# Kernel tuning notes

Measured on AMD Instinct MI355X. Metric: run time of the kernel, lower is better.

## Reference

```python
import jax, jax.numpy as jnp
import numpy as np

E = 8      # num_experts
A = 128    # angle feature size = input_size - 4
TGT = 3    # target size
HID = 16   # expert MLP hidden / latent / main GRU hidden
OUT = 128  # motion decoder output size
B = 64
W = 128
F = A + TGT + 1  # 132
BN_EPS = 1e-5


def _gru_layer(x, Wih, Whh, bih, bhh):
    # x: (B, T, I); Wih: (3H, I); Whh: (3H, H). PyTorch GRU equations.
    xW = jnp.einsum('bti,gi->btg', x, Wih) + bih  # precompute input gates (B,T,3H)
    H = Whh.shape[1]

    def step(h, xw):
        gh = h @ Whh.T + bhh
        ir, iz, inn = jnp.split(xw, 3, axis=-1)
        hr, hz, hn = jnp.split(gh, 3, axis=-1)
        r = jax.nn.sigmoid(ir + hr)
        z = jax.nn.sigmoid(iz + hz)
        n = jnp.tanh(inn + r * hn)
        h_new = (1.0 - z) * n + z * h
        return h_new, h_new

    h0 = jnp.zeros((x.shape[0], H), x.dtype)
    _, ys = jax.lax.scan(step, h0, jnp.swapaxes(xW, 0, 1))
    return jnp.swapaxes(ys, 0, 1)  # (B, T, H)


def _expert_mlp(x, om, w1, b1, w2, b2, g, bt):
    # Blend expert weights per-sample, then matvec; fused as one einsum (same math).
    h = jnp.einsum('bi,be,eih->bh', x, om, w1) + om @ b1
    # BatchNorm1d, training-mode batch statistics (biased variance), then ELU
    m = h.mean(0)
    v = h.var(0)
    h = jax.nn.elu(g * (h - m) * jax.lax.rsqrt(v + BN_EPS) + bt)
    return jnp.einsum('bh,be,eho->bo', h, om, w2) + om @ b2


def _forward(Local, Remote,
             gW_ih0, gW_hh0, gb_ih0, gb_hh0, gW_ih1, gW_hh1, gb_ih1, gb_hh1,
             ae_w1, ae_b1, ae_w2, ae_b2, ae_g, ae_bt,
             md_w1, md_b1, md_w2, md_b2, md_g, md_bt,
             mW_ih0, mW_hh0, mb_ih0, mb_hh0, mW_ih1, mW_hh1, mb_ih1, mb_hh1):
    Bn, Wn, _ = Local.shape
    LA = Local[..., :A]
    RA = Remote[..., :A]
    LT = Local[..., A:A + TGT]
    RT = Remote[..., A:A + TGT]
    Scale = Remote[..., A + TGT]  # (B, W)

    def gate(t):
        h = _gru_layer(t, gW_ih0, gW_hh0, gb_ih0, gb_hh0)
        h = _gru_layer(h, gW_ih1, gW_hh1, gb_ih1, gb_hh1)
        return jax.nn.softmax(h, axis=-1)

    Lo = gate(LT)  # (B, W, E)
    Ro = gate(RT)

    ZL = _expert_mlp(LA.reshape(-1, A), Lo.reshape(-1, E), ae_w1, ae_b1, ae_w2, ae_b2, ae_g, ae_bt)
    ZR = _expert_mlp(RA.reshape(-1, A), Ro.reshape(-1, E), ae_w1, ae_b1, ae_w2, ae_b2, ae_g, ae_bt)
    Z = (ZL + ZR).reshape(Bn, Wn, HID)

    Z = _gru_layer(Z, mW_ih0, mW_hh0, mb_ih0, mb_hh0)
    Z = _gru_layer(Z, mW_ih1, mW_hh1, mb_ih1, mb_hh1)
    Z = Z[:, -1]  # (B, HID)

    dec_in = jnp.concatenate([Z, Scale[:, -1:]], axis=-1)  # (B, HID+1)
    return _expert_mlp(dec_in, Ro[:, -1], md_w1, md_b1, md_w2, md_b2, md_g, md_bt)


def setup_inputs() -> dict:
    key = jax.random.key(0)
    ks = iter(jax.random.split(key, 40))

    def u(shape, bound):
        return jax.random.uniform(next(ks), shape, jnp.float32, -bound, bound)

    d = {}
    d['Local'] = jax.random.normal(next(ks), (B, W, F), jnp.float32)
    d['Remote'] = jax.random.normal(next(ks), (B, W, F), jnp.float32)

    def gru_params(pref, isz, hsz):
        bd = 1.0 / np.sqrt(hsz)
        d[pref + 'W_ih0'] = u((3 * hsz, isz), bd)
        d[pref + 'W_hh0'] = u((3 * hsz, hsz), bd)
        d[pref + 'b_ih0'] = u((3 * hsz,), bd)
        d[pref + 'b_hh0'] = u((3 * hsz,), bd)
        d[pref + 'W_ih1'] = u((3 * hsz, hsz), bd)
        d[pref + 'W_hh1'] = u((3 * hsz, hsz), bd)
        d[pref + 'b_ih1'] = u((3 * hsz,), bd)
        d[pref + 'b_hh1'] = u((3 * hsz,), bd)

    gru_params('g', TGT, E)    # gating GRU: 2 layers, hidden = num_experts
    gru_params('m', HID, HID)  # main GRU: 2 layers, hidden = 16

    def expert(pref, isz, hsz, osz):
        b1 = float(np.sqrt(6.0 / (isz * hsz)))
        b2 = float(np.sqrt(6.0 / (hsz * osz)))
        d[pref + '_w1'] = u((E, isz, hsz), b1)
        d[pref + '_b1'] = jnp.zeros((E, hsz), jnp.float32)
        d[pref + '_w2'] = u((E, hsz, osz), b2)
        d[pref + '_b2'] = jnp.zeros((E, osz), jnp.float32)
        d[pref + '_g'] = jnp.ones((hsz,), jnp.float32)
        d[pref + '_bt'] = jnp.zeros((hsz,), jnp.float32)

    expert('ae', A, HID, HID)        # angle encoder
    expert('md', HID + 1, HID, OUT)  # motion decoder
    return d


def reference(Local, Remote,
              gW_ih0, gW_hh0, gb_ih0, gb_hh0, gW_ih1, gW_hh1, gb_ih1, gb_hh1,
              ae_w1, ae_b1, ae_w2, ae_b2, ae_g, ae_bt,
              md_w1, md_b1, md_w2, md_b2, md_g, md_bt,
              mW_ih0, mW_hh0, mb_ih0, mb_hh0, mW_ih1, mW_hh1, mb_ih1, mb_hh1):
    return _forward(Local, Remote,
                    gW_ih0, gW_hh0, gb_ih0, gb_hh0, gW_ih1, gW_hh1, gb_ih1, gb_hh1,
                    ae_w1, ae_b1, ae_w2, ae_b2, ae_g, ae_bt,
                    md_w1, md_b1, md_w2, md_b2, md_g, md_bt,
                    mW_ih0, mW_hh0, mb_ih0, mb_hh0, mW_ih1, mW_hh1, mb_ih1, mb_hh1)
```

## Files before the change

kernel.cpp:

```cpp
#include <hip/hip_runtime.h>
#include <cstdint>
#include <cstddef>

#define DEV __device__ __forceinline__

typedef float v2f __attribute__((ext_vector_type(2)));

DEV float fsig(float x)  { return __builtin_amdgcn_rcpf(1.0f + __expf(-x)); }
DEV float ftanh_(float x){ return 1.0f - 2.0f * __builtin_amdgcn_rcpf(1.0f + __expf(2.0f * x)); }
DEV float readlanef(float v, int l) {
    return __uint_as_float(__builtin_amdgcn_readlane(__float_as_uint(v), l));
}
DEV v2f fma2v(v2f a, float b, v2f c) {
    return (v2f){ fmaf(a.x, b, c.x), fmaf(a.y, b, c.y) };
}

constexpr size_t ACC   = 0;
constexpr size_t LO    = 128;
constexpr size_t RO    = LO + 65536;
constexpr size_t HBUF  = RO + 65536;
constexpr size_t XW0   = HBUF + 262144;
constexpr size_t ZLAST = XW0 + 393216;

__global__ __launch_bounds__(64) void k1_gate(
    const float* __restrict__ Local, const float* __restrict__ Remote,
    const float* __restrict__ Wih0, const float* __restrict__ Whh0,
    const float* __restrict__ bih0, const float* __restrict__ bhh0,
    const float* __restrict__ Wih1, const float* __restrict__ Whh1,
    const float* __restrict__ bih1, const float* __restrict__ bhh1,
    float* __restrict__ ws)
{
    const int tid = threadIdx.x;
    const int j = tid & 7;
    const int layer = (tid >> 3) & 1;
    const int blk = blockIdx.x;
    const int track = blk >> 6;
    const int b = blk & 63;
    if (blk == 0) ws[ACC + tid] = 0.f;

    __shared__ float xwg[128][24];
    __shared__ float h1all[128][9];

    const float* __restrict__ src = track ? Remote : Local;
    for (int t = tid; t < 128; t += 64) {
        const float* p = src + ((size_t)b * 128 + t) * 132 + 128;
        float x0 = p[0], x1 = p[1], x2 = p[2];
#pragma unroll
        for (int u = 0; u < 24; ++u) {
            float a = bih0[u];
            a = fmaf(Wih0[u * 3 + 0], x0, a);
            a = fmaf(Wih0[u * 3 + 1], x1, a);
            a = fmaf(Wih0[u * 3 + 2], x2, a);
            xwg[t][u] = a;
        }
    }

    v2f wrz[16], wnn[16];
    float base_r, base_z, base_in, base_dn;
    if (layer == 0) {
#pragma unroll
        for (int k = 0; k < 8; ++k) {
            wrz[k] = (v2f){ Whh0[j * 8 + k], Whh0[(8 + j) * 8 + k] };
            wnn[k] = (v2f){ 0.f, Whh0[(16 + j) * 8 + k] };
            wrz[8 + k] = (v2f){0.f, 0.f};
            wnn[8 + k] = (v2f){0.f, 0.f};
        }
        base_r = bhh0[j];
        base_z = bhh0[8 + j];
        base_in = 0.f;
        base_dn = bhh0[16 + j];
    } else {
#pragma unroll
        for (int k = 0; k < 8; ++k) {
            wrz[k] = (v2f){ Wih1[j * 8 + k], Wih1[(8 + j) * 8 + k] };
            wnn[k] = (v2f){ Wih1[(16 + j) * 8 + k], 0.f };
            wrz[8 + k] = (v2f){ Whh1[j * 8 + k], Whh1[(8 + j) * 8 + k] };
            wnn[8 + k] = (v2f){ 0.f, Whh1[(16 + j) * 8 + k] };
        }
        base_r = bih1[j] + bhh1[j];
        base_z = bih1[8 + j] + bhh1[8 + j];
        base_in = bih1[16 + j];
        base_dn = bhh1[16 + j];
    }
    const float m0f = (layer == 0) ? 1.f : 0.f;
    __syncthreads();

    float hown = 0.f;
    float p0 = xwg[0][j], p1 = xwg[0][8 + j], p2 = xwg[0][16 + j];
#pragma unroll 1
    for (int t = 0; t <= 128; ++t) {
        int tn = t < 127 ? t + 1 : 127;
        float q0 = xwg[tn][j], q1 = xwg[tn][8 + j], q2 = xwg[tn][16 + j];
        float vb[16];
#pragma unroll
        for (int k = 0; k < 16; ++k) vb[k] = readlanef(hown, k);
        v2f arz = (v2f){ fmaf(m0f, p0, base_r), fmaf(m0f, p1, base_z) };
        v2f ann = (v2f){ fmaf(m0f, p2, base_in), base_dn };
#pragma unroll
        for (int k = 0; k < 16; ++k) {
            arz = fma2v(wrz[k], vb[k], arz);
            ann = fma2v(wnn[k], vb[k], ann);
        }
        float r = fsig(arz.x);
        float z = fsig(arz.y);
        float n = ftanh_(ann.x + r * ann.y);
        float hnew = (1.f - z) * n + z * hown;
        bool act = layer ? (t >= 1) : (t < 128);
        hown = act ? hnew : hown;
        if (tid >= 8 && tid < 16 && t >= 1) h1all[t - 1][j] = hown;
        p0 = q0; p1 = q1; p2 = q2;
    }
    __syncthreads();

    float* __restrict__ outp = ws + (track ? RO : LO);
    for (int t = tid; t < 128; t += 64) {
        float vv[8];
#pragma unroll
        for (int k = 0; k < 8; ++k) vv[k] = h1all[t][k];
        float mx = vv[0];
#pragma unroll
        for (int k = 1; k < 8; ++k) mx = fmaxf(mx, vv[k]);
        float ssum = 0.f;
#pragma unroll
        for (int k = 0; k < 8; ++k) { vv[k] = __expf(vv[k] - mx); ssum += vv[k]; }
        float inv = __builtin_amdgcn_rcpf(ssum);
        size_t base = ((size_t)b * 128 + t) * 8;
        float4 o0 = make_float4(vv[0] * inv, vv[1] * inv, vv[2] * inv, vv[3] * inv);
        float4 o1 = make_float4(vv[4] * inv, vv[5] * inv, vv[6] * inv, vv[7] * inv);
        *(float4*)(outp + base) = o0;
        *(float4*)(outp + base + 4) = o1;
    }
}

__global__ __launch_bounds__(256) void k2_expert1(
    const float* __restrict__ Local, const float* __restrict__ Remote,
    const float* __restrict__ ae_w1, const float* __restrict__ ae_b1,
    float* __restrict__ ws)
{
    const int blk = blockIdx.x;
    const int track = blk >> 7;
    const int n0 = (blk & 127) * 64;
    const float* __restrict__ X = track ? Remote : Local;
    const float* __restrict__ om = ws + (track ? RO : LO);

    __shared__ __align__(16) float xsh[64 * 132];
    __shared__ __align__(16) float wsh[16 * 1040];
    __shared__ float omsh[64][8];
    __shared__ float b1sh[128];
    __shared__ float red[32];
    const int tid = threadIdx.x;

    for (int i = tid; i < 2048; i += 256) {
        int r = i >> 5, q = i & 31;
        ((float4*)&xsh[r * 132])[q] = ((const float4*)(X + (size_t)(n0 + r) * 132))[q];
    }
    for (int i4 = tid; i4 < 4096; i4 += 256) {
        float4 v = ((const float4*)ae_w1)[i4];
        int i = i4 * 4;
#pragma unroll
        for (int c = 0; c < 4; ++c) {
            int ii = i + c;
            int h = ii & 15, kk = (ii >> 4) & 127, e = ii >> 11;
            float vc = c == 0 ? v.x : c == 1 ? v.y : c == 2 ? v.z : v.w;
            wsh[h * 1040 + e * 130 + kk] = vc;
        }
    }
    for (int i = tid; i < 512; i += 256) omsh[i >> 3][i & 7] = om[(size_t)(n0 + (i >> 3)) * 8 + (i & 7)];
    for (int i = tid; i < 128; i += 256) b1sh[i] = ae_b1[i];
    if (tid < 32) red[tid] = 0.f;
    __syncthreads();

    const int hh = tid & 15, rg = tid >> 4;
    float acc[4][8];
#pragma unroll
    for (int r = 0; r < 4; ++r)
#pragma unroll
        for (int e = 0; e < 8; ++e) acc[r][e] = 0.f;

#pragma unroll 4
    for (int kq = 0; kq < 32; ++kq) {
        float4 xv[4], wv[8];
#pragma unroll
        for (int r = 0; r < 4; ++r) xv[r] = *(const float4*)&xsh[(rg * 4 + r) * 132 + kq * 4];
#pragma unroll
        for (int e = 0; e < 8; ++e) wv[e] = *(const float4*)&wsh[hh * 1040 + e * 130 + kq * 4];
#pragma unroll
        for (int r = 0; r < 4; ++r)
#pragma unroll
            for (int e = 0; e < 8; ++e) {
                float a = acc[r][e];
                a = fmaf(xv[r].x, wv[e].x, a);
                a = fmaf(xv[r].y, wv[e].y, a);
                a = fmaf(xv[r].z, wv[e].z, a);
                a = fmaf(xv[r].w, wv[e].w, a);
                acc[r][e] = a;
            }
    }

    float s = 0.f, s2 = 0.f;
    float* __restrict__ hout = ws + HBUF + (size_t)track * 131072;
#pragma unroll
    for (int r = 0; r < 4; ++r) {
        int row = rg * 4 + r;
        float hv = 0.f;
#pragma unroll
        for (int e = 0; e < 8; ++e) hv = fmaf(omsh[row][e], acc[r][e] + b1sh[e * 16 + hh], hv);
        hout[(size_t)(n0 + row) * 16 + hh] = hv;
        s += hv; s2 += hv * hv;
    }
    __syncthreads();
    atomicAdd(&red[hh], s);
    atomicAdd(&red[16 + hh], s2);
    __syncthreads();
    if (tid < 32) atomicAdd(&ws[ACC + track * 32 + tid], red[tid]);
}

__global__ __launch_bounds__(256) void k3_bn_mlp2(
    const float* __restrict__ ae_w2, const float* __restrict__ ae_b2,
    const float* __restrict__ ae_g, const float* __restrict__ ae_bt,
    const float* __restrict__ mWih0, const float* __restrict__ mbih0,
    float* __restrict__ ws)
{
    const int n0 = blockIdx.x * 64;
    const int tid = threadIdx.x;
    __shared__ float actsh[2][64][16];
    __shared__ float omsh[2][64][8];
    __shared__ float w2sh[2048];
    __shared__ float b2sh[128];
    __shared__ float zsh[64][17];
    __shared__ float wihsh[48][17];
    __shared__ float bihsh[48];
    __shared__ float stat[4][16];

    if (tid < 32) {
        int trk = tid >> 4, h = tid & 15;
        float s = ws[ACC + trk * 32 + h], s2 = ws[ACC + trk * 32 + 16 + h];
        float m = s * (1.f / 8192.f);
        float v = fmaxf(s2 * (1.f / 8192.f) - m * m, 0.f);
        stat[trk * 2][h] = m;
        stat[trk * 2 + 1][h] = rsqrtf(v + 1e-5f);
    }
    for (int i = tid; i < 2048; i += 256) w2sh[i] = ae_w2[i];
    for (int i = tid; i < 128; i += 256) b2sh[i] = ae_b2[i];
    for (int i = tid; i < 768; i += 256) wihsh[i >> 4][i & 15] = mWih0[i];
    if (tid < 48) bihsh[tid] = mbih0[tid];
    for (int i = tid; i < 1024; i += 256) {
        int trk = i >> 9, r = (i >> 3) & 63, e = i & 7;
        omsh[trk][r][e] = ws[(trk ? RO : LO) + (size_t)(n0 + r) * 8 + e];
    }
    __syncthreads();

    for (int i = tid; i < 2048; i += 256) {
        int trk = i >> 10, r = (i >> 4) & 63, h = i & 15;
        float v = ws[HBUF + (size_t)trk * 131072 + (size_t)(n0 + r) * 16 + h];
        float a = ae_g[h] * (v - stat[trk * 2][h]) * stat[trk * 2 + 1][h] + ae_bt[h];
        actsh[trk][r][h] = a > 0.f ? a : expm1f(a);
    }
    __syncthreads();

    for (int i = tid; i < 1024; i += 256) {
        int r = i >> 4, o = i & 15;
        float accv = 0.f;
#pragma unroll
        for (int trk = 0; trk < 2; ++trk) {
#pragma unroll
            for (int e = 0; e < 8; ++e) {
                const float* w = &w2sh[e * 256 + o];
                float t = b2sh[e * 16 + o];
#pragma unroll
                for (int h = 0; h < 16; ++h) t = fmaf(actsh[trk][r][h], w[h * 16], t);
                accv = fmaf(omsh[trk][r][e], t, accv);
            }
        }
        zsh[r][o] = accv;
    }
    __syncthreads();

    for (int i = tid; i < 3072; i += 256) {
        int r = i / 48, gr = i - r * 48;
        float a = bihsh[gr];
#pragma unroll
        for (int k = 0; k < 16; ++k) a = fmaf(zsh[r][k], wihsh[gr][k], a);
        ws[XW0 + (size_t)(n0 + r) * 48 + gr] = a;
    }
}

__global__ __launch_bounds__(64) void k4_maingru(
    const float* __restrict__ Whh0, const float* __restrict__ bhh0,
    const float* __restrict__ Wih1, const float* __restrict__ Whh1,
    const float* __restrict__ bih1, const float* __restrict__ bhh1,
    float* __restrict__ ws)
{
    const int tid = threadIdx.x;
    const int j = tid & 15;
    const int layer = (tid >> 4) & 1;
    const int seq = blockIdx.x;

    __shared__ __align__(16) float4 xw4[1536];
    float* xwsh = (float*)xw4;

    const float4* __restrict__ xsrc = (const float4*)(ws + XW0 + (size_t)seq * 6144);
    for (int i = tid; i < 1536; i += 64) xw4[i] = xsrc[i];

    v2f wrz[32], wnn[32];
    float base_r, base_z, base_in, base_dn;
    if (layer == 0) {
#pragma unroll
        for (int k = 0; k < 16; ++k) {
            wrz[k] = (v2f){ Whh0[j * 16 + k], Whh0[(16 + j) * 16 + k] };
            wnn[k] = (v2f){ 0.f, Whh0[(32 + j) * 16 + k] };
            wrz[16 + k] = (v2f){0.f, 0.f};
            wnn[16 + k] = (v2f){0.f, 0.f};
        }
        base_r = bhh0[j];
        base_z = bhh0[16 + j];
        base_in = 0.f;
        base_dn = bhh0[32 + j];
    } else {
#pragma unroll
        for (int k = 0; k < 16; ++k) {
            wrz[k] = (v2f){ Wih1[j * 16 + k], Wih1[(16 + j) * 16 + k] };
            wnn[k] = (v2f){ Wih1[(32 + j) * 16 + k], 0.f };
            wrz[16 + k] = (v2f){ Whh1[j * 16 + k], Whh1[(16 + j) * 16 + k] };
            wnn[16 + k] = (v2f){ 0.f, Whh1[(32 + j) * 16 + k] };
        }
        base_r = bih1[j] + bhh1[j];
        base_z = bih1[16 + j] + bhh1[16 + j];
        base_in = bih1[32 + j];
        base_dn = bhh1[32 + j];
    }
    const float m0f = (layer == 0) ? 1.f : 0.f;
    __syncthreads();

    float hown = 0.f;
    float p0 = xwsh[j], p1 = xwsh[16 + j], p2 = xwsh[32 + j];
#pragma unroll 1
    for (int t = 0; t <= 128; ++t) {
        int tn = (t < 127 ? t + 1 : 127) * 48;
        float q0 = xwsh[tn + j], q1 = xwsh[tn + 16 + j], q2 = xwsh[tn + 32 + j];
        float vb[32];
#pragma unroll
        for (int k = 0; k < 32; ++k) vb[k] = readlanef(hown, k);
        v2f arz = (v2f){ fmaf(m0f, p0, base_r), fmaf(m0f, p1, base_z) };
        v2f ann = (v2f){ fmaf(m0f, p2, base_in), base_dn };
#pragma unroll
        for (int k = 0; k < 32; ++k) {
            arz = fma2v(wrz[k], vb[k], arz);
            ann = fma2v(wnn[k], vb[k], ann);
        }
        float r = fsig(arz.x);
        float z = fsig(arz.y);
        float n = ftanh_(ann.x + r * ann.y);
        float hnew = (1.f - z) * n + z * hown;
        bool act = layer ? (t >= 1) : (t < 128);
        hown = act ? hnew : hown;
        p0 = q0; p1 = q1; p2 = q2;
    }
    if (tid >= 16 && tid < 32) ws[ZLAST + (size_t)seq * 16 + j] = hown;
}

__global__ __launch_bounds__(256) void k5_dec(
    const float* __restrict__ Remote,
    const float* __restrict__ md_w1, const float* __restrict__ md_b1,
    const float* __restrict__ md_g, const float* __restrict__ md_bt,
    const float* __restrict__ md_w2, const float* __restrict__ md_b2,
    const float* __restrict__ ws, float* __restrict__ out)
{
    const int o0 = blockIdx.x * 8;
    const int tid = threadIdx.x;
    __shared__ float xsh[64][17];
    __shared__ float omsh[64][8];
    __shared__ float w1sh[2176];
    __shared__ float b1sh[128];
    __shared__ float hsh[64][17];
    __shared__ float ssum[16], ss2[16], mstat[2][16];
    __shared__ float ash[64][17];
    __shared__ float w2sh[8][16][8];
    __shared__ float b2sh[8][8];

    for (int i = tid; i < 1024; i += 256) xsh[i >> 4][i & 15] = ws[ZLAST + i];
    if (tid < 64) xsh[tid][16] = Remote[((size_t)tid * 128 + 127) * 132 + 131];
    for (int i = tid; i < 512; i += 256)
        omsh[i >> 3][i & 7] = ws[RO + ((size_t)(i >> 3) * 128 + 127) * 8 + (i & 7)];
    for (int i = tid; i < 2176; i += 256) w1sh[i] = md_w1[i];
    for (int i = tid; i < 128; i += 256) b1sh[i] = md_b1[i];
    for (int i = tid; i < 1024; i += 256) {
        int e = i >> 7, h = (i >> 3) & 15, oo = i & 7;
        w2sh[e][h][oo] = md_w2[((size_t)e * 16 + h) * 128 + o0 + oo];
    }
    if (tid < 64) b2sh[tid >> 3][tid & 7] = md_b2[(size_t)(tid >> 3) * 128 + o0 + (tid & 7)];
    if (tid < 16) { ssum[tid] = 0.f; ss2[tid] = 0.f; }
    __syncthreads();

    for (int i = tid; i < 1024; i += 256) {
        int b = i >> 4, h = i & 15;
        float accv = 0.f;
#pragma unroll
        for (int e = 0; e < 8; ++e) {
            float t = b1sh[e * 16 + h];
            const float* w = &w1sh[e * 272 + h];
#pragma unroll
            for (int i2 = 0; i2 < 17; ++i2) t = fmaf(xsh[b][i2], w[i2 * 16], t);
            accv = fmaf(omsh[b][e], t, accv);
        }
        hsh[b][h] = accv;
        atomicAdd(&ssum[h], accv);
        atomicAdd(&ss2[h], accv * accv);
    }
    __syncthreads();
    if (tid < 16) {
        float m = ssum[tid] * (1.f / 64.f);
// ... 9 lines not shown
    }
    __syncthreads();

    for (int i = tid; i < 512; i += 256) {
        int b = i >> 3, oo = i & 7;
        float accv = 0.f;
#pragma unroll
        for (int e = 0; e < 8; ++e) {
            float t = b2sh[e][oo];
#pragma unroll
            for (int h = 0; h < 16; ++h) t = fmaf(ash[b][h], w2sh[e][h][oo], t);
            accv = fmaf(omsh[b][e], t, accv);
        }
        out[(size_t)b * 128 + o0 + oo] = accv;
    }
}

extern "C" void kernel_launch(void* const* d_in, const int* in_sizes, int n_in,
                              void* d_out, int out_size, void* d_ws, size_t ws_size,
                              hipStream_t stream) {
    const float* Local  = (const float*)d_in[0];
    const float* Remote = (const float*)d_in[1];
    const float* gWih0  = (const float*)d_in[2];
    const float* gWhh0  = (const float*)d_in[3];
    const float* gbih0  = (const float*)d_in[4];
    const float* gbhh0  = (const float*)d_in[5];
    const float* gWih1  = (const float*)d_in[6];
    const float* gWhh1  = (const float*)d_in[7];
    const float* gbih1  = (const float*)d_in[8];
    const float* gbhh1  = (const float*)d_in[9];
    const float* mWih0  = (const float*)d_in[10];
    const float* mWhh0  = (const float*)d_in[11];
    const float* mbih0  = (const float*)d_in[12];
    const float* mbhh0  = (const float*)d_in[13];
    const float* mWih1  = (const float*)d_in[14];
    const float* mWhh1  = (const float*)d_in[15];
    const float* mbih1  = (const float*)d_in[16];
    const float* mbhh1  = (const float*)d_in[17];
    const float* ae_w1  = (const float*)d_in[18];
    const float* ae_b1  = (const float*)d_in[19];
    const float* ae_w2  = (const float*)d_in[20];
    const float* ae_b2  = (const float*)d_in[21];
    const float* ae_g   = (const float*)d_in[22];
    const float* ae_bt  = (const float*)d_in[23];
    const float* md_w1  = (const float*)d_in[24];
    const float* md_b1  = (const float*)d_in[25];
    const float* md_w2  = (const float*)d_in[26];
    const float* md_b2  = (const float*)d_in[27];
    const float* md_g   = (const float*)d_in[28];
    const float* md_bt  = (const float*)d_in[29];
    float* ws  = (float*)d_ws;
    float* out = (float*)d_out;

    k1_gate<<<128, 64, 0, stream>>>(Local, Remote, gWih0, gWhh0, gbih0, gbhh0,
                                    gWih1, gWhh1, gbih1, gbhh1, ws);
    k2_expert1<<<256, 256, 0, stream>>>(Local, Remote, ae_w1, ae_b1, ws);
    k3_bn_mlp2<<<128, 256, 0, stream>>>(ae_w2, ae_b2, ae_g, ae_bt, mWih0, mbih0, ws);
    k4_maingru<<<64, 64, 0, stream>>>(mWhh0, mbhh0, mWih1, mWhh1, mbih1, mbhh1, ws);
    k5_dec<<<16, 256, 0, stream>>>(Remote, md_w1, md_b1, md_g, md_bt,
                                   md_w2, md_b2, ws, out);
}
```

Before: 264.9 us.

## Fuse BN/expert-MLP2 with main GRU and split GRU dot products into independent chains

Merges the BatchNorm/ELU/second expert layer and input-gate projection kernel with the main GRU recurrence kernel, so each block computes its sequence's input gates directly into shared memory instead of round-tripping through global workspace, removing one launch. The GRU inner loops in both the gate and main GRU kernels replace packed v2f accumulators with six scalar FMA chains split by half of the hidden vector, shortening dependency chains on the serial critical path. The fused kernel uses only 64 of 256 threads for the recurrence and needs more shared memory per block, and only 64 blocks do the MLP work that 128 blocks did before.

```diff
diff --git a/kernel.cpp b/kernel.cpp
--- a/kernel.cpp
+++ b/kernel.cpp
@@ -3,26 +3,20 @@
 #include <cstddef>
 
 #define DEV __device__ __forceinline__
-
-typedef float v2f __attribute__((ext_vector_type(2)));
 
 DEV float fsig(float x)  { return __builtin_amdgcn_rcpf(1.0f + __expf(-x)); }
 DEV float ftanh_(float x){ return 1.0f - 2.0f * __builtin_amdgcn_rcpf(1.0f + __expf(2.0f * x)); }
 DEV float readlanef(float v, int l) {
     return __uint_as_float(__builtin_amdgcn_readlane(__float_as_uint(v), l));
 }
-DEV v2f fma2v(v2f a, float b, v2f c) {
-    return (v2f){ fmaf(a.x, b, c.x), fmaf(a.y, b, c.y) };
-}
 
 constexpr size_t ACC   = 0;
 constexpr size_t LO    = 128;
 constexpr size_t RO    = LO + 65536;
 constexpr size_t HBUF  = RO + 65536;
-constexpr size_t XW0   = HBUF + 262144;
-constexpr size_t ZLAST = XW0 + 393216;
-
-__global__ __launch_bounds__(64) void k1_gate(
+constexpr size_t ZLAST = HBUF + 262144;
+
+__global__ __launch_bounds__(64, 1) void k1_gate(
     const float* __restrict__ Local, const float* __restrict__ Remote,
     const float* __restrict__ Wih0, const float* __restrict__ Whh0,
     const float* __restrict__ bih0, const float* __restrict__ bhh0,
@@ -55,34 +49,23 @@
         }
     }
 
-    v2f wrz[16], wnn[16];
-    float base_r, base_z, base_in, base_dn;
-    if (layer == 0) {
-#pragma unroll
-        for (int k = 0; k < 8; ++k) {
-            wrz[k] = (v2f){ Whh0[j * 8 + k], Whh0[(8 + j) * 8 + k] };
-            wnn[k] = (v2f){ 0.f, Whh0[(16 + j) * 8 + k] };
-            wrz[8 + k] = (v2f){0.f, 0.f};
-            wnn[8 + k] = (v2f){0.f, 0.f};
-        }
-        base_r = bhh0[j];
-        base_z = bhh0[8 + j];
-        base_in = 0.f;
-        base_dn = bhh0[16 + j];
-    } else {
-#pragma unroll
-        for (int k = 0; k < 8; ++k) {
-            wrz[k] = (v2f){ Wih1[j * 8 + k], Wih1[(8 + j) * 8 + k] };
-            wnn[k] = (v2f){ Wih1[(16 + j) * 8 + k], 0.f };
-            wrz[8 + k] = (v2f){ Whh1[j * 8 + k], Whh1[(8 + j) * 8 + k] };
-            wnn[8 + k] = (v2f){ 0.f, Whh1[(16 + j) * 8 + k] };
-        }
-        base_r = bih1[j] + bhh1[j];
-        base_z = bih1[8 + j] + bhh1[8 + j];
-        base_in = bih1[16 + j];
-        base_dn = bhh1[16 + j];
-    }
-    const float m0f = (layer == 0) ? 1.f : 0.f;
+    const float* __restrict__ Wlo = layer ? Wih1 : Whh0;
+    const float mhi = layer ? 1.f : 0.f;
+    const float m0f = layer ? 0.f : 1.f;
+    float wr[16], wz[16], wc[16];
+#pragma unroll
+    for (int k = 0; k < 8; ++k) {
+        wr[k] = Wlo[j * 8 + k];
+        wz[k] = Wlo[(8 + j) * 8 + k];
+        wc[k] = Wlo[(16 + j) * 8 + k];
+        wr[8 + k] = mhi * Whh1[j * 8 + k];
+        wz[8 + k] = mhi * Whh1[(8 + j) * 8 + k];
+        wc[8 + k] = mhi * Whh1[(16 + j) * 8 + k];
+    }
+    const float base_r  = layer ? (bih1[j] + bhh1[j])         : bhh0[j];
+    const float base_z  = layer ? (bih1[8 + j] + bhh1[8 + j]) : bhh0[8 + j];
+    const float base_in = layer ? bih1[16 + j]                : 0.f;
+    const float base_dn = layer ? bhh1[16 + j]                : bhh0[16 + j];
     __syncthreads();
 
     float hown = 0.f;
@@ -94,16 +77,24 @@
         float vb[16];
 #pragma unroll
         for (int k = 0; k < 16; ++k) vb[k] = readlanef(hown, k);
-        v2f arz = (v2f){ fmaf(m0f, p0, base_r), fmaf(m0f, p1, base_z) };
-        v2f ann = (v2f){ fmaf(m0f, p2, base_in), base_dn };
-#pragma unroll
-        for (int k = 0; k < 16; ++k) {
-            arz = fma2v(wrz[k], vb[k], arz);
-            ann = fma2v(wnn[k], vb[k], ann);
-        }
-        float r = fsig(arz.x);
-        float z = fsig(arz.y);
-        float n = ftanh_(ann.x + r * ann.y);
+        float ar_a = fmaf(m0f, p0, base_r), ar_b = 0.f;
+        float az_a = fmaf(m0f, p1, base_z), az_b = 0.f;
+        float ac_lo = 0.f, ac_hi = 0.f;
+#pragma unroll
+        for (int k = 0; k < 8; ++k) {
+            ar_a  = fmaf(wr[k], vb[k], ar_a);
+            az_a  = fmaf(wz[k], vb[k], az_a);
+            ac_lo = fmaf(wc[k], vb[k], ac_lo);
+            ar_b  = fmaf(wr[8 + k], vb[8 + k], ar_b);
+            az_b  = fmaf(wz[8 + k], vb[8 + k], az_b);
+            ac_hi = fmaf(wc[8 + k], vb[8 + k], ac_hi);
+        }
+        float r = fsig(ar_a + ar_b);
+        float z = fsig(az_a + az_b);
+        float tin = base_in + ac_lo;
+        float in_ = layer ? tin : p2;
+        float dn  = base_dn + (layer ? ac_hi : ac_lo);
+        float n = ftanh_(in_ + r * dn);
         float hnew = (1.f - z) * n + z * hown;
         bool act = layer ? (t >= 1) : (t < 128);
         hown = act ? hnew : hown;
@@ -215,122 +206,103 @@
     if (tid < 32) atomicAdd(&ws[ACC + track * 32 + tid], red[tid]);
 }
 
-__global__ __launch_bounds__(256) void k3_bn_mlp2(
+__global__ __launch_bounds__(256, 1) void k34_fused(
     const float* __restrict__ ae_w2, const float* __restrict__ ae_b2,
     const float* __restrict__ ae_g, const float* __restrict__ ae_bt,
     const float* __restrict__ mWih0, const float* __restrict__ mbih0,
-    float* __restrict__ ws)
-{
-    const int n0 = blockIdx.x * 64;
-    const int tid = threadIdx.x;
-    __shared__ float actsh[2][64][16];
-    __shared__ float omsh[2][64][8];
-    __shared__ float w2sh[2048];
-    __shared__ float b2sh[128];
-    __shared__ float zsh[64][17];
-    __shared__ float wihsh[48][17];
-    __shared__ float bihsh[48];
-    __shared__ float stat[4][16];
-
-    if (tid < 32) {
-        int trk = tid >> 4, h = tid & 15;
-        float s = ws[ACC + trk * 32 + h], s2 = ws[ACC + trk * 32 + 16 + h];
-        float m = s * (1.f / 8192.f);
-        float v = fmaxf(s2 * (1.f / 8192.f) - m * m, 0.f);
-        stat[trk * 2][h] = m;
-        stat[trk * 2 + 1][h] = rsqrtf(v + 1e-5f);
-    }
-    for (int i = tid; i < 2048; i += 256) w2sh[i] = ae_w2[i];
-    for (int i = tid; i < 128; i += 256) b2sh[i] = ae_b2[i];
-    for (int i = tid; i < 768; i += 256) wihsh[i >> 4][i & 15] = mWih0[i];
-    if (tid < 48) bihsh[tid] = mbih0[tid];
-    for (int i = tid; i < 1024; i += 256) {
-        int trk = i >> 9, r = (i >> 3) & 63, e = i & 7;
-        omsh[trk][r][e] = ws[(trk ? RO : LO) + (size_t)(n0 + r) * 8 + e];
-    }
-    __syncthreads();
-
-    for (int i = tid; i < 2048; i += 256) {
-        int trk = i >> 10, r = (i >> 4) & 63, h = i & 15;
-        float v = ws[HBUF + (size_t)trk * 131072 + (size_t)(n0 + r) * 16 + h];
-        float a = ae_g[h] * (v - stat[trk * 2][h]) * stat[trk * 2 + 1][h] + ae_bt[h];
-        actsh[trk][r][h] = a > 0.f ? a : expm1f(a);
-    }
-    __syncthreads();
-
-    for (int i = tid; i < 1024; i += 256) {
-        int r = i >> 4, o = i & 15;
-        float accv = 0.f;
-#pragma unroll
-        for (int trk = 0; trk < 2; ++trk) {
-#pragma unroll
-            for (int e = 0; e < 8; ++e) {
-                const float* w = &w2sh[e * 256 + o];
-                float t = b2sh[e * 16 + o];
-#pragma unroll
-                for (int h = 0; h < 16; ++h) t = fmaf(actsh[trk][r][h], w[h * 16], t);
-                accv = fmaf(omsh[trk][r][e], t, accv);
-            }
-        }
-        zsh[r][o] = accv;
-    }
-    __syncthreads();
-
-    for (int i = tid; i < 3072; i += 256) {
-        int r = i / 48, gr = i - r * 48;
-        float a = bihsh[gr];
-#pragma unroll
-        for (int k = 0; k < 16; ++k) a = fmaf(zsh[r][k], wihsh[gr][k], a);
-        ws[XW0 + (size_t)(n0 + r) * 48 + gr] = a;
-    }
-}
-
-__global__ __launch_bounds__(64) void k4_maingru(
     const float* __restrict__ Whh0, const float* __restrict__ bhh0,
     const float* __restrict__ Wih1, const float* __restrict__ Whh1,
     const float* __restrict__ bih1, const float* __restrict__ bhh1,
     float* __restrict__ ws)
 {
+    const int s = blockIdx.x;
     const int tid = threadIdx.x;
+
+    __shared__ float stat[4][16];
+    __shared__ float omsh[2][128][8];
+    __shared__ float w2sh[2048];
+    __shared__ float b2sh[128];
+    __shared__ float actsh[2][128][16];
+    __shared__ float zsh[128][17];
+    __shared__ float wihsh[48][17];
+    __shared__ float bihsh[48];
+    __shared__ float xwsh[128 * 48];
+
+    if (tid < 32) {
+        int trk = tid >> 4, h = tid & 15;
+        float sm = ws[ACC + trk * 32 + h], s2 = ws[ACC + trk * 32 + 16 + h];
+        float m = sm * (1.f / 8192.f);
+        float v = fmaxf(s2 * (1.f / 8192.f) - m * m, 0.f);
+        stat[trk * 2][h] = m;
+        stat[trk * 2 + 1][h] = rsqrtf(v + 1e-5f);
+    }
+    for (int i = tid; i < 2048; i += 256) w2sh[i] = ae_w2[i];
+    for (int i = tid; i < 128; i += 256) b2sh[i] = ae_b2[i];
+    for (int i = tid; i < 768; i += 256) wihsh[i >> 4][i & 15] = mWih0[i];
+    if (tid < 48) bihsh[tid] = mbih0[tid];
+    for (int i = tid; i < 2048; i += 256) {
+        int trk = i >> 10, r = (i >> 3) & 127, e = i & 7;
+        omsh[trk][r][e] = ws[(trk ? RO : LO) + ((size_t)s * 128 + r) * 8 + e];
+    }
+    __syncthreads();
+
+    for (int i = tid; i < 4096; i += 256) {
+        int trk = i >> 11, r = (i >> 4) & 127, h = i & 15;
+        float v = ws[HBUF + (size_t)trk * 131072 + ((size_t)s * 128 + r) * 16 + h];
+        float a = ae_g[h] * (v - stat[trk * 2][h]) * stat[trk * 2 + 1][h] + ae_bt[h];
+        actsh[trk][r][h] = a > 0.f ? a : expm1f(a);
+    }
+    __syncthreads();
+
+    for (int i = tid; i < 2048; i += 256) {
+        int r = i >> 4, o = i & 15;
+        float accv = 0.f;
+#pragma unroll
+        for (int trk = 0; trk < 2; ++trk) {
+#pragma unroll
+            for (int e = 0; e < 8; ++e) {
+                const float* w = &w2sh[e * 256 + o];
+                float t = b2sh[e * 16 + o];
+#pragma unroll
+                for (int h = 0; h < 16; ++h) t = fmaf(actsh[trk][r][h], w[h * 16], t);
+                accv = fmaf(omsh[trk][r][e], t, accv);
+            }
+        }
+        zsh[r][o] = accv;
+    }
+    __syncthreads();
+
+    for (int i = tid; i < 6144; i += 256) {
+        int r = i / 48, g = i - r * 48;
+        float a = bihsh[g];
+#pragma unroll
+        for (int k = 0; k < 16; ++k) a = fmaf(zsh[r][k], wihsh[g][k], a);
+        xwsh[r * 48 + g] = a;
+    }
+    __syncthreads();
+
+    if (tid >= 64) return;
+
     const int j = tid & 15;
     const int layer = (tid >> 4) & 1;
-    const int seq = blockIdx.x;
-
-    __shared__ __align__(16) float4 xw4[1536];
-    float* xwsh = (float*)xw4;
-
-    const float4* __restrict__ xsrc = (const float4*)(ws + XW0 + (size_t)seq * 6144);
-    for (int i = tid; i < 1536; i += 64) xw4[i] = xsrc[i];
-
-    v2f wrz[32], wnn[32];
-    float base_r, base_z, base_in, base_dn;
-    if (layer == 0) {
-#pragma unroll
-        for (int k = 0; k < 16; ++k) {
-            wrz[k] = (v2f){ Whh0[j * 16 + k], Whh0[(16 + j) * 16 + k] };
-            wnn[k] = (v2f){ 0.f, Whh0[(32 + j) * 16 + k] };
-            wrz[16 + k] = (v2f){0.f, 0.f};
-            wnn[16 + k] = (v2f){0.f, 0.f};
-        }
-        base_r = bhh0[j];
-        base_z = bhh0[16 + j];
-        base_in = 0.f;
-        base_dn = bhh0[32 + j];
-    } else {
-#pragma unroll
-        for (int k = 0; k < 16; ++k) {
-            wrz[k] = (v2f){ Wih1[j * 16 + k], Wih1[(16 + j) * 16 + k] };
-            wnn[k] = (v2f){ Wih1[(32 + j) * 16 + k], 0.f };
-            wrz[16 + k] = (v2f){ Whh1[j * 16 + k], Whh1[(16 + j) * 16 + k] };
-            wnn[16 + k] = (v2f){ 0.f, Whh1[(32 + j) * 16 + k] };
-        }
-        base_r = bih1[j] + bhh1[j];
-        base_z = bih1[16 + j] + bhh1[16 + j];
-        base_in = bih1[32 + j];
-        base_dn = bhh1[32 + j];
-    }
-    const float m0f = (layer == 0) ? 1.f : 0.f;
-    __syncthreads();
+
+    const float* __restrict__ Wlo = layer ? Wih1 : Whh0;
+    const float mhi = layer ? 1.f : 0.f;
+    const float m0f = layer ? 0.f : 1.f;
+    float wr[32], wz[32], wc[32];
+#pragma unroll
+    for (int k = 0; k < 16; ++k) {
+        wr[k] = Wlo[j * 16 + k];
+        wz[k] = Wlo[(16 + j) * 16 + k];
+        wc[k] = Wlo[(32 + j) * 16 + k];
+        wr[16 + k] = mhi * Whh1[j * 16 + k];
+        wz[16 + k] = mhi * Whh1[(16 + j) * 16 + k];
+        wc[16 + k] = mhi * Whh1[(32 + j) * 16 + k];
+    }
+    const float base_r  = layer ? (bih1[j] + bhh1[j])           : bhh0[j];
+    const float base_z  = layer ? (bih1[16 + j] + bhh1[16 + j]) : bhh0[16 + j];
+    const float base_in = layer ? bih1[32 + j]                  : 0.f;
+    const float base_dn = layer ? bhh1[32 + j]                  : bhh0[32 + j];
 
     float hown = 0.f;
     float p0 = xwsh[j], p1 = xwsh[16 + j], p2 = xwsh[32 + j];
@@ -341,22 +313,30 @@
         float vb[32];
 #pragma unroll
         for (int k = 0; k < 32; ++k) vb[k] = readlanef(hown, k);
-        v2f arz = (v2f){ fmaf(m0f, p0, base_r), fmaf(m0f, p1, base_z) };
-        v2f ann = (v2f){ fmaf(m0f, p2, base_in), base_dn };
-#pragma unroll
-        for (int k = 0; k < 32; ++k) {
-            arz = fma2v(wrz[k], vb[k], arz);
-            ann = fma2v(wnn[k], vb[k], ann);
-        }
-        float r = fsig(arz.x);
-        float z = fsig(arz.y);
-        float n = ftanh_(ann.x + r * ann.y);
+        float ar_a = fmaf(m0f, p0, base_r), ar_b = 0.f;
+        float az_a = fmaf(m0f, p1, base_z), az_b = 0.f;
+        float ac_lo = 0.f, ac_hi = 0.f;
+#pragma unroll
+        for (int k = 0; k < 16; ++k) {
+            ar_a  = fmaf(wr[k], vb[k], ar_a);
+            az_a  = fmaf(wz[k], vb[k], az_a);
+            ac_lo = fmaf(wc[k], vb[k], ac_lo);
+            ar_b  = fmaf(wr[16 + k], vb[16 + k], ar_b);
+            az_b  = fmaf(wz[16 + k], vb[16 + k], az_b);
+            ac_hi = fmaf(wc[16 + k], vb[16 + k], ac_hi);
+        }
+        float r = fsig(ar_a + ar_b);
+        float z = fsig(az_a + az_b);
+        float tin = base_in + ac_lo;
+        float in_ = layer ? tin : p2;
+        float dn  = base_dn + (layer ? ac_hi : ac_lo);
+        float n = ftanh_(in_ + r * dn);
         float hnew = (1.f - z) * n + z * hown;
         bool act = layer ? (t >= 1) : (t < 128);
         hown = act ? hnew : hown;
         p0 = q0; p1 = q1; p2 = q2;
     }
-    if (tid >= 16 && tid < 32) ws[ZLAST + (size_t)seq * 16 + j] = hown;
+    if (tid >= 16 && tid < 32) ws[ZLAST + (size_t)s * 16 + j] = hown;
 }
 
 __global__ __launch_bounds__(256) void k5_dec(
@@ -475,8 +455,8 @@
     k1_gate<<<128, 64, 0, stream>>>(Local, Remote, gWih0, gWhh0, gbih0, gbhh0,
                                     gWih1, gWhh1, gbih1, gbhh1, ws);
     k2_expert1<<<256, 256, 0, stream>>>(Local, Remote, ae_w1, ae_b1, ws);
-    k3_bn_mlp2<<<128, 256, 0, stream>>>(ae_w2, ae_b2, ae_g, ae_bt, mWih0, mbih0, ws);
-    k4_maingru<<<64, 64, 0, stream>>>(mWhh0, mbhh0, mWih1, mWhh1, mbih1, mbhh1, ws);
+    k34_fused<<<64, 256, 0, stream>>>(ae_w2, ae_b2, ae_g, ae_bt, mWih0, mbih0,
+                                      mWhh0, mbhh0, mWih1, mWhh1, mbih1, mbhh1, ws);
     k5_dec<<<16, 256, 0, stream>>>(Remote, md_w1, md_b1, md_g, md_bt,
                                    md_w2, md_b2, ws, out);
 }
```

After: 246.6 us. 6.9% less time.

## Batch GRU recurrences across sequences with split-f16 MFMA matmuls

Applied to the files above, without the earlier changes.

Rewrites the gate GRU and main GRU kernels so each wave processes 16 sequences at once. The per-step recurrent matvecs become 16x16x16 f16 MFMAs, with weights and hidden states split into hi/lo halves to keep near-fp32 precision. This replaces the serial readlane broadcast and FMA chain, and the gate kernel now fuses the input projection and softmax into the step loop. Far fewer blocks are launched, and each step has a long dependent MFMA chain whose latency may dominate.

```diff
diff --git a/kernel.cpp b/kernel.cpp
--- a/kernel.cpp
+++ b/kernel.cpp
@@ -4,15 +4,28 @@
 
 #define DEV __device__ __forceinline__
 
-typedef float v2f __attribute__((ext_vector_type(2)));
+typedef _Float16 v4h __attribute__((ext_vector_type(4)));
+typedef float    v4f __attribute__((ext_vector_type(4)));
 
 DEV float fsig(float x)  { return __builtin_amdgcn_rcpf(1.0f + __expf(-x)); }
 DEV float ftanh_(float x){ return 1.0f - 2.0f * __builtin_amdgcn_rcpf(1.0f + __expf(2.0f * x)); }
-DEV float readlanef(float v, int l) {
-    return __uint_as_float(__builtin_amdgcn_readlane(__float_as_uint(v), l));
-}
-DEV v2f fma2v(v2f a, float b, v2f c) {
-    return (v2f){ fmaf(a.x, b, c.x), fmaf(a.y, b, c.y) };
+DEV float swz16f(float v) {
+    return __uint_as_float(__builtin_amdgcn_ds_swizzle(__float_as_uint(v), 0x401F));
+}
+#define MFMA(a, b, c) __builtin_amdgcn_mfma_f32_16x16x16f16((a), (b), (c), 0, 0, 0)
+#define LND(x) asm volatile("" : "+v"(x))
+
+DEV v4h cvt_hi(v4f x) {
+    v4h r;
+#pragma unroll
+    for (int i = 0; i < 4; ++i) r[i] = (_Float16)x[i];
+    return r;
+}
+DEV v4h cvt_lo(v4f x, v4h hi) {
+    v4h r;
+#pragma unroll
+    for (int i = 0; i < 4; ++i) r[i] = (_Float16)(x[i] - (float)hi[i]);
+    return r;
 }
 
 constexpr size_t ACC   = 0;
@@ -22,7 +35,7 @@
 constexpr size_t XW0   = HBUF + 262144;
 constexpr size_t ZLAST = XW0 + 393216;
 
-__global__ __launch_bounds__(64) void k1_gate(
+__global__ __launch_bounds__(64, 1) void k1_gate(
     const float* __restrict__ Local, const float* __restrict__ Remote,
     const float* __restrict__ Wih0, const float* __restrict__ Whh0,
     const float* __restrict__ bih0, const float* __restrict__ bhh0,
@@ -31,104 +44,120 @@
     float* __restrict__ ws)
 {
     const int tid = threadIdx.x;
-    const int j = tid & 7;
-    const int layer = (tid >> 3) & 1;
     const int blk = blockIdx.x;
-    const int track = blk >> 6;
-    const int b = blk & 63;
+    const int track = blk >> 2;
+    const int b0 = (blk & 3) * 16;
+    const int n_ = tid & 15;
+    const int m  = tid & 15;
+    const int kq = (tid >> 4) * 4;
     if (blk == 0) ws[ACC + tid] = 0.f;
 
-    __shared__ float xwg[128][24];
-    __shared__ float h1all[128][9];
+    __shared__ __align__(16) float4 xs4[128 * 16];
 
     const float* __restrict__ src = track ? Remote : Local;
-    for (int t = tid; t < 128; t += 64) {
-        const float* p = src + ((size_t)b * 128 + t) * 132 + 128;
-        float x0 = p[0], x1 = p[1], x2 = p[2];
-#pragma unroll
-        for (int u = 0; u < 24; ++u) {
-            float a = bih0[u];
-            a = fmaf(Wih0[u * 3 + 0], x0, a);
-            a = fmaf(Wih0[u * 3 + 1], x1, a);
-            a = fmaf(Wih0[u * 3 + 2], x2, a);
-            xwg[t][u] = a;
-        }
-    }
-
-    v2f wrz[16], wnn[16];
-    float base_r, base_z, base_in, base_dn;
-    if (layer == 0) {
-#pragma unroll
-        for (int k = 0; k < 8; ++k) {
-            wrz[k] = (v2f){ Whh0[j * 8 + k], Whh0[(8 + j) * 8 + k] };
-            wnn[k] = (v2f){ 0.f, Whh0[(16 + j) * 8 + k] };
-            wrz[8 + k] = (v2f){0.f, 0.f};
-            wnn[8 + k] = (v2f){0.f, 0.f};
-        }
-        base_r = bhh0[j];
-        base_z = bhh0[8 + j];
-        base_in = 0.f;
-        base_dn = bhh0[16 + j];
-    } else {
-#pragma unroll
-        for (int k = 0; k < 8; ++k) {
-            wrz[k] = (v2f){ Wih1[j * 8 + k], Wih1[(8 + j) * 8 + k] };
-            wnn[k] = (v2f){ Wih1[(16 + j) * 8 + k], 0.f };
-            wrz[8 + k] = (v2f){ Whh1[j * 8 + k], Whh1[(8 + j) * 8 + k] };
-            wnn[8 + k] = (v2f){ 0.f, Whh1[(16 + j) * 8 + k] };
-        }
-        base_r = bih1[j] + bhh1[j];
-        base_z = bih1[8 + j] + bhh1[8 + j];
-        base_in = bih1[16 + j];
-        base_dn = bhh1[16 + j];
-    }
-    const float m0f = (layer == 0) ? 1.f : 0.f;
-    __syncthreads();
-
-    float hown = 0.f;
-    float p0 = xwg[0][j], p1 = xwg[0][8 + j], p2 = xwg[0][16 + j];
+    for (int i = tid; i < 2048; i += 64) {
+        int t = i >> 4, n = i & 15;
+        const float* p = src + ((size_t)(b0 + n) * 128 + t) * 132 + 128;
+        xs4[t * 16 + n] = make_float4(p[0], p[1], p[2], 0.f);
+    }
+
+    v4f f_rh, f_zh, f_ci, f_ch, f_rx, f_zx, f_cx;
+#pragma unroll
+    for (int i = 0; i < 4; ++i) {
+        int k = kq + i;
+        float rh, zh, ci, ch;
+        if (m < 8) {
+            rh = (k < 8) ? Whh0[m * 8 + k] : 0.f;
+            zh = (k < 8) ? Whh0[(8 + m) * 8 + k] : 0.f;
+            ci = 0.f;
+            ch = (k < 8) ? Whh0[(16 + m) * 8 + k] : 0.f;
+        } else {
+            int j = m - 8;
+            rh = (k < 8) ? Wih1[j * 8 + k] : Whh1[j * 8 + (k - 8)];
+            zh = (k < 8) ? Wih1[(8 + j) * 8 + k] : Whh1[(8 + j) * 8 + (k - 8)];
+            ci = (k < 8) ? Wih1[(16 + j) * 8 + k] : 0.f;
+            ch = (k >= 8) ? Whh1[(16 + j) * 8 + (k - 8)] : 0.f;
+        }
+        f_rh[i] = rh; f_zh[i] = zh; f_ci[i] = ci; f_ch[i] = ch;
+        bool xon = (m < 8) && (k < 3);
+        f_rx[i] = xon ? Wih0[m * 3 + k] : 0.f;
+        f_zx[i] = xon ? Wih0[(8 + m) * 3 + k] : 0.f;
+        f_cx[i] = xon ? Wih0[(16 + m) * 3 + k] : 0.f;
+    }
+    v4h a_rh_hi = cvt_hi(f_rh), a_rh_lo = cvt_lo(f_rh, a_rh_hi);
+    v4h a_zh_hi = cvt_hi(f_zh), a_zh_lo = cvt_lo(f_zh, a_zh_hi);
+    v4h a_ci_hi = cvt_hi(f_ci), a_ci_lo = cvt_lo(f_ci, a_ci_hi);
+    v4h a_ch_hi = cvt_hi(f_ch), a_ch_lo = cvt_lo(f_ch, a_ch_hi);
+    v4h a_rx_hi = cvt_hi(f_rx), a_rx_lo = cvt_lo(f_rx, a_rx_hi);
+    v4h a_zx_hi = cvt_hi(f_zx), a_zx_lo = cvt_lo(f_zx, a_zx_hi);
+    v4h a_cx_hi = cvt_hi(f_cx), a_cx_lo = cvt_lo(f_cx, a_cx_hi);
+    LND(a_rh_hi); LND(a_rh_lo); LND(a_zh_hi); LND(a_zh_lo);
+    LND(a_ci_hi); LND(a_ci_lo); LND(a_ch_hi); LND(a_ch_lo);
+    LND(a_rx_hi); LND(a_rx_lo); LND(a_zx_hi); LND(a_zx_lo);
+    LND(a_cx_hi); LND(a_cx_lo);
+
+    v4f c_r, c_z, c_ci, c_ch;
+#pragma unroll
+    for (int i = 0; i < 4; ++i) {
+        int mc = kq + i;
+        if (mc < 8) {
+            c_r[i]  = bih0[mc] + bhh0[mc];
+            c_z[i]  = bih0[8 + mc] + bhh0[8 + mc];
+            c_ci[i] = bih0[16 + mc];
+            c_ch[i] = bhh0[16 + mc];
+        } else {
+            int j = mc - 8;
+            c_r[i]  = bih1[j] + bhh1[j];
+            c_z[i]  = bih1[8 + j] + bhh1[8 + j];
+            c_ci[i] = bih1[16 + j];
+            c_ch[i] = bhh1[16 + j];
+        }
+    }
+    LND(c_r); LND(c_z); LND(c_ci); LND(c_ch);
+    __syncthreads();
+
+    float* __restrict__ outp = ws + (track ? RO : LO);
+    const bool hi_half = (tid >= 32);
+
+    v4f h = {0.f, 0.f, 0.f, 0.f};
+    float4 xc = xs4[n_];
 #pragma unroll 1
     for (int t = 0; t <= 128; ++t) {
-        int tn = t < 127 ? t + 1 : 127;
-        float q0 = xwg[tn][j], q1 = xwg[tn][8 + j], q2 = xwg[tn][16 + j];
-        float vb[16];
-#pragma unroll
-        for (int k = 0; k < 16; ++k) vb[k] = readlanef(hown, k);
-        v2f arz = (v2f){ fmaf(m0f, p0, base_r), fmaf(m0f, p1, base_z) };
-        v2f ann = (v2f){ fmaf(m0f, p2, base_in), base_dn };
-#pragma unroll
-        for (int k = 0; k < 16; ++k) {
-            arz = fma2v(wrz[k], vb[k], arz);
-            ann = fma2v(wnn[k], vb[k], ann);
-        }
-        float r = fsig(arz.x);
-        float z = fsig(arz.y);
-        float n = ftanh_(ann.x + r * ann.y);
-        float hnew = (1.f - z) * n + z * hown;
-        bool act = layer ? (t >= 1) : (t < 128);
-        hown = act ? hnew : hown;
-        if (tid >= 8 && tid < 16 && t >= 1) h1all[t - 1][j] = hown;
-        p0 = q0; p1 = q1; p2 = q2;
-    }
-    __syncthreads();
-
-    float* __restrict__ outp = ws + (track ? RO : LO);
-    for (int t = tid; t < 128; t += 64) {
-        float vv[8];
-#pragma unroll
-        for (int k = 0; k < 8; ++k) vv[k] = h1all[t][k];
-        float mx = vv[0];
-#pragma unroll
-        for (int k = 1; k < 8; ++k) mx = fmaxf(mx, vv[k]);
-        float ssum = 0.f;
-#pragma unroll
-        for (int k = 0; k < 8; ++k) { vv[k] = __expf(vv[k] - mx); ssum += vv[k]; }
-        float inv = __builtin_amdgcn_rcpf(ssum);
-        size_t base = ((size_t)b * 128 + t) * 8;
-        float4 o0 = make_float4(vv[0] * inv, vv[1] * inv, vv[2] * inv, vv[3] * inv);
-        float4 o1 = make_float4(vv[4] * inv, vv[5] * inv, vv[6] * inv, vv[7] * inv);
-        *(float4*)(outp + base) = o0;
-        *(float4*)(outp + base + 4) = o1;
+        float4 xn = xs4[(t < 127 ? t + 1 : 127) * 16 + n_];
+        v4h bh_hi = cvt_hi(h), bh_lo = cvt_lo(h, bh_hi);
+        v4f xv = {xc.x, xc.y, xc.z, 0.f};
+        v4h bx_hi = cvt_hi(xv), bx_lo = cvt_lo(xv, bx_hi);
+
+        v4f Dr = c_r, Dz = c_z, Dci = c_ci, Dch = c_ch;
+        Dr = MFMA(a_rh_hi, bh_hi, Dr); Dr = MFMA(a_rh_hi, bh_lo, Dr); Dr = MFMA(a_rh_lo, bh_hi, Dr);
+        Dr = MFMA(a_rx_hi, bx_hi, Dr); Dr = MFMA(a_rx_hi, bx_lo, Dr); Dr = MFMA(a_rx_lo, bx_hi, Dr);
+        Dz = MFMA(a_zh_hi, bh_hi, Dz); Dz = MFMA(a_zh_hi, bh_lo, Dz); Dz = MFMA(a_zh_lo, bh_hi, Dz);
+        Dz = MFMA(a_zx_hi, bx_hi, Dz); Dz = MFMA(a_zx_hi, bx_lo, Dz); Dz = MFMA(a_zx_lo, bx_hi, Dz);
+        Dci = MFMA(a_ci_hi, bh_hi, Dci); Dci = MFMA(a_ci_hi, bh_lo, Dci); Dci = MFMA(a_ci_lo, bh_hi, Dci);
+        Dci = MFMA(a_cx_hi, bx_hi, Dci); Dci = MFMA(a_cx_hi, bx_lo, Dci); Dci = MFMA(a_cx_lo, bx_hi, Dci);
+        Dch = MFMA(a_ch_hi, bh_hi, Dch); Dch = MFMA(a_ch_hi, bh_lo, Dch); Dch = MFMA(a_ch_lo, bh_hi, Dch);
+
+        bool act = hi_half ? (t >= 1) : (t < 128);
+#pragma unroll
+        for (int i = 0; i < 4; ++i) {
+            float r = fsig(Dr[i]);
+            float z = fsig(Dz[i]);
+            float n = ftanh_(Dci[i] + r * Dch[i]);
+            float hv = n + z * (h[i] - n);
+            h[i] = act ? hv : h[i];
+        }
+
+        if (t >= 1) {
+            float e0 = __expf(h[0]), e1 = __expf(h[1]), e2 = __expf(h[2]), e3 = __expf(h[3]);
+            float ps = e0 + e1 + e2 + e3;
+            float po = swz16f(ps);
+            float inv = __builtin_amdgcn_rcpf(ps + po);
+            if (hi_half) {
+                float4 o = make_float4(e0 * inv, e1 * inv, e2 * inv, e3 * inv);
+                *(float4*)(outp + ((size_t)(b0 + n_) * 128 + (t - 1)) * 8 + (kq - 8)) = o;
+            }
+        }
+        xc = xn;
     }
 }
 
@@ -285,78 +314,99 @@
     }
 }
 
-__global__ __launch_bounds__(64) void k4_maingru(
+__global__ __launch_bounds__(64, 1) void k4_maingru(
     const float* __restrict__ Whh0, const float* __restrict__ bhh0,
     const float* __restrict__ Wih1, const float* __restrict__ Whh1,
     const float* __restrict__ bih1, const float* __restrict__ bhh1,
     float* __restrict__ ws)
 {
     const int tid = threadIdx.x;
-    const int j = tid & 15;
-    const int layer = (tid >> 4) & 1;
-    const int seq = blockIdx.x;
-
-    __shared__ __align__(16) float4 xw4[1536];
-    float* xwsh = (float*)xw4;
-
-    const float4* __restrict__ xsrc = (const float4*)(ws + XW0 + (size_t)seq * 6144);
-    for (int i = tid; i < 1536; i += 64) xw4[i] = xsrc[i];
-
-    v2f wrz[32], wnn[32];
-    float base_r, base_z, base_in, base_dn;
-    if (layer == 0) {
-#pragma unroll
-        for (int k = 0; k < 16; ++k) {
-            wrz[k] = (v2f){ Whh0[j * 16 + k], Whh0[(16 + j) * 16 + k] };
-            wnn[k] = (v2f){ 0.f, Whh0[(32 + j) * 16 + k] };
-            wrz[16 + k] = (v2f){0.f, 0.f};
-            wnn[16 + k] = (v2f){0.f, 0.f};
-        }
-        base_r = bhh0[j];
-        base_z = bhh0[16 + j];
-        base_in = 0.f;
-        base_dn = bhh0[32 + j];
-    } else {
-#pragma unroll
-        for (int k = 0; k < 16; ++k) {
-            wrz[k] = (v2f){ Wih1[j * 16 + k], Wih1[(16 + j) * 16 + k] };
-            wnn[k] = (v2f){ Wih1[(32 + j) * 16 + k], 0.f };
-            wrz[16 + k] = (v2f){ Whh1[j * 16 + k], Whh1[(16 + j) * 16 + k] };
-            wnn[16 + k] = (v2f){ 0.f, Whh1[(32 + j) * 16 + k] };
-        }
-        base_r = bih1[j] + bhh1[j];
-        base_z = bih1[16 + j] + bhh1[16 + j];
-        base_in = bih1[32 + j];
-        base_dn = bhh1[32 + j];
-    }
-    const float m0f = (layer == 0) ? 1.f : 0.f;
-    __syncthreads();
-
-    float hown = 0.f;
-    float p0 = xwsh[j], p1 = xwsh[16 + j], p2 = xwsh[32 + j];
+    const int seqbase = blockIdx.x * 16;
+    const int n_ = tid & 15;
+    const int m  = tid & 15;
+    const int kq = (tid >> 4) * 4;
+
+    v4f f;
+#define FRAG(name, W, rowbase) \
+    { float4 w4 = *(const float4*)&(W)[((rowbase) + m) * 16 + kq]; \
+      f[0] = w4.x; f[1] = w4.y; f[2] = w4.z; f[3] = w4.w; } \
+    v4h name##_hi = cvt_hi(f); v4h name##_lo = cvt_lo(f, name##_hi); \
+    LND(name##_hi); LND(name##_lo);
+    FRAG(a_rh0, Whh0, 0)
+    FRAG(a_zh0, Whh0, 16)
+    FRAG(a_ch0, Whh0, 32)
+    FRAG(a_ri1, Wih1, 0)
+    FRAG(a_rh1, Whh1, 0)
+    FRAG(a_zi1, Wih1, 16)
+    FRAG(a_zh1, Whh1, 16)
+    FRAG(a_ci1, Wih1, 32)
+    FRAG(a_ch1, Whh1, 32)
+#undef FRAG
+
+    v4f c_r0, c_z0, c_ch0, c_r1, c_z1, c_ci1, c_ch1;
+#pragma unroll
+    for (int i = 0; i < 4; ++i) {
+        int mc = kq + i;
+        c_r0[i]  = bhh0[mc];
+        c_z0[i]  = bhh0[16 + mc];
+        c_ch0[i] = bhh0[32 + mc];
+        c_r1[i]  = bih1[mc] + bhh1[mc];
+        c_z1[i]  = bih1[16 + mc] + bhh1[16 + mc];
+        c_ci1[i] = bih1[32 + mc];
+        c_ch1[i] = bhh1[32 + mc];
+    }
+    LND(c_r0); LND(c_z0); LND(c_ch0); LND(c_r1); LND(c_z1); LND(c_ci1); LND(c_ch1);
+
+    const float* __restrict__ xwb = ws + XW0 + (size_t)(seqbase + n_) * 128 * 48 + kq;
+    float4 xr = *(const float4*)(xwb + 0);
+    float4 xz = *(const float4*)(xwb + 16);
+    float4 xn2 = *(const float4*)(xwb + 32);
+
+    v4f h0 = {0.f, 0.f, 0.f, 0.f};
+    v4f h1 = {0.f, 0.f, 0.f, 0.f};
 #pragma unroll 1
     for (int t = 0; t <= 128; ++t) {
         int tn = (t < 127 ? t + 1 : 127) * 48;
-        float q0 = xwsh[tn + j], q1 = xwsh[tn + 16 + j], q2 = xwsh[tn + 32 + j];
-        float vb[32];
-#pragma unroll
-        for (int k = 0; k < 32; ++k) vb[k] = readlanef(hown, k);
-        v2f arz = (v2f){ fmaf(m0f, p0, base_r), fmaf(m0f, p1, base_z) };
-        v2f ann = (v2f){ fmaf(m0f, p2, base_in), base_dn };
-#pragma unroll
-        for (int k = 0; k < 32; ++k) {
-            arz = fma2v(wrz[k], vb[k], arz);
-            ann = fma2v(wnn[k], vb[k], ann);
-        }
-        float r = fsig(arz.x);
-        float z = fsig(arz.y);
-        float n = ftanh_(ann.x + r * ann.y);
-        float hnew = (1.f - z) * n + z * hown;
-        bool act = layer ? (t >= 1) : (t < 128);
-        hown = act ? hnew : hown;
-        p0 = q0; p1 = q1; p2 = q2;
-    }
-    if (tid >= 16 && tid < 32) ws[ZLAST + (size_t)seq * 16 + j] = hown;
+        float4 qr = *(const float4*)(xwb + tn);
+        float4 qz = *(const float4*)(xwb + tn + 16);
+        float4 qc = *(const float4*)(xwb + tn + 32);
+
+        v4h b0_hi = cvt_hi(h0), b0_lo = cvt_lo(h0, b0_hi);
+        v4h b1_hi = cvt_hi(h1), b1_lo = cvt_lo(h1, b1_hi);
+
+        v4f Dr0 = c_r0, Dz0 = c_z0, Dch0 = c_ch0;
+        v4f Dr1 = c_r1, Dz1 = c_z1, Dci1 = c_ci1, Dch1 = c_ch1;
+        Dr0 = MFMA(a_rh0_hi, b0_hi, Dr0); Dr0 = MFMA(a_rh0_hi, b0_lo, Dr0); Dr0 = MFMA(a_rh0_lo, b0_hi, Dr0);
+        Dz0 = MFMA(a_zh0_hi, b0_hi, Dz0); Dz0 = MFMA(a_zh0_hi, b0_lo, Dz0); Dz0 = MFMA(a_zh0_lo, b0_hi, Dz0);
+        Dch0 = MFMA(a_ch0_hi, b0_hi, Dch0); Dch0 = MFMA(a_ch0_hi, b0_lo, Dch0); Dch0 = MFMA(a_ch0_lo, b0_hi, Dch0);
+        Dr1 = MFMA(a_ri1_hi, b0_hi, Dr1); Dr1 = MFMA(a_ri1_hi, b0_lo, Dr1); Dr1 = MFMA(a_ri1_lo, b0_hi, Dr1);
+        Dr1 = MFMA(a_rh1_hi, b1_hi, Dr1); Dr1 = MFMA(a_rh1_hi, b1_lo, Dr1); Dr1 = MFMA(a_rh1_lo, b1_hi, Dr1);
+        Dz1 = MFMA(a_zi1_hi, b0_hi, Dz1); Dz1 = MFMA(a_zi1_hi, b0_lo, Dz1); Dz1 = MFMA(a_zi1_lo, b0_hi, Dz1);
+        Dz1 = MFMA(a_zh1_hi, b1_hi, Dz1); Dz1 = MFMA(a_zh1_hi, b1_lo, Dz1); Dz1 = MFMA(a_zh1_lo, b1_hi, Dz1);
+        Dci1 = MFMA(a_ci1_hi, b0_hi, Dci1); Dci1 = MFMA(a_ci1_hi, b0_lo, Dci1); Dci1 = MFMA(a_ci1_lo, b0_hi, Dci1);
+        Dch1 = MFMA(a_ch1_hi, b1_hi, Dch1); Dch1 = MFMA(a_ch1_hi, b1_lo, Dch1); Dch1 = MFMA(a_ch1_lo, b1_hi, Dch1);
+
+        bool act0 = (t < 128), act1 = (t >= 1);
+        float xrv[4] = {xr.x, xr.y, xr.z, xr.w};
+        float xzv[4] = {xz.x, xz.y, xz.z, xz.w};
+        float xcv[4] = {xn2.x, xn2.y, xn2.z, xn2.w};
+#pragma unroll
+        for (int i = 0; i < 4; ++i) {
+            float r0 = fsig(Dr0[i] + xrv[i]);
+            float z0 = fsig(Dz0[i] + xzv[i]);
+            float n0 = ftanh_(xcv[i] + r0 * Dch0[i]);
+            float h0v = n0 + z0 * (h0[i] - n0);
+            h0[i] = act0 ? h0v : h0[i];
+            float r1 = fsig(Dr1[i]);
+            float z1 = fsig(Dz1[i]);
+            float n1 = ftanh_(Dci1[i] + r1 * Dch1[i]);
+            float h1v = n1 + z1 * (h1[i] - n1);
+            h1[i] = act1 ? h1v : h1[i];
+        }
+        xr = qr; xz = qz; xn2 = qc;
+    }
+    float4 o = make_float4(h1[0], h1[1], h1[2], h1[3]);
+    *(float4*)(ws + ZLAST + (size_t)(seqbase + n_) * 16 + kq) = o;
 }
 
 __global__ __launch_bounds__(256) void k5_dec(
@@ -472,11 +522,11 @@
     float* ws  = (float*)d_ws;
     float* out = (float*)d_out;
 
-    k1_gate<<<128, 64, 0, stream>>>(Local, Remote, gWih0, gWhh0, gbih0, gbhh0,
-                                    gWih1, gWhh1, gbih1, gbhh1, ws);
+    k1_gate<<<8, 64, 0, stream>>>(Local, Remote, gWih0, gWhh0, gbih0, gbhh0,
+                                  gWih1, gWhh1, gbih1, gbhh1, ws);
     k2_expert1<<<256, 256, 0, stream>>>(Local, Remote, ae_w1, ae_b1, ws);
     k3_bn_mlp2<<<128, 256, 0, stream>>>(ae_w2, ae_b2, ae_g, ae_bt, mWih0, mbih0, ws);
-    k4_maingru<<<64, 64, 0, stream>>>(mWhh0, mbhh0, mWih1, mWhh1, mbih1, mbhh1, ws);
+    k4_maingru<<<4, 64, 0, stream>>>(mWhh0, mbhh0, mWih1, mWhh1, mbih1, mbhh1, ws);
     k5_dec<<<16, 256, 0, stream>>>(Remote, md_w1, md_b1, md_g, md_bt,
                                    md_w2, md_b2, ws, out);
 }
```

Result: slower. 355.1 us (+34.1%).
